# Optimization experiments

Measured on AMD Instinct MI355X. Metric: run time of the kernel, lower is better.

## Reference

```python
import jax, jax.numpy as jnp
import numpy as np

B, CIN, HIN, WIN = 1, 26, 721, 1440
K, HOUT, KH, KW = 9, 360, 9, 9
COUT = 256
PSCALE = WIN // (WIN // 2)  # lon downsample stride = 2
WOUT = WIN // 2


def setup_inputs() -> dict:
    key = jax.random.key(0)
    k1, k2, k3 = jax.random.split(key, 3)
    x = jax.random.normal(k1, (B, CIN, HIN, WIN), dtype=jnp.float32)
    # precomputed basis*quadrature stencil psi[k, ho, dh, dw] (shift-invariant in lon,
    # stored only for wo=0, exactly as DISCO does). Normalized per (k, ho) ('mean' mode).
    psi = jax.random.normal(k2, (K, HOUT, KH, KW), dtype=jnp.float32)
    psi = psi / (jnp.mean(jnp.abs(psi), axis=(2, 3), keepdims=True) * (KH * KW) + 1e-6)
    weight = jax.random.normal(k3, (COUT, CIN, K), dtype=jnp.float32) * (1.0 / np.sqrt(CIN * K))
    # base input-lat row for each output lat (stencil top row), clipped to valid range
    hi_base = np.clip(np.round(np.arange(HOUT) * (HIN - 1) / HOUT).astype(np.int32) - KH // 2, 0, HIN - 1)
    return {"x": x, "psi": psi, "weight": weight, "hi_base": jnp.asarray(hi_base, dtype=jnp.int32)}


def _disco_conv(x, psi, weight, hi_base):
    x = x.astype(jnp.float32)  # fp32 autocast-off region, matches torch module
    acc = jnp.zeros((B, CIN, K, HOUT, WOUT), dtype=jnp.float32)
    for dh in range(KH):  # small structural loop over stencil rows
        rows = jnp.clip(hi_base + dh, 0, HIN - 1)  # [Hout]
        xr = x[:, :, rows, :]
        for dw in range(KW):  # small structural loop over stencil lon offsets
            shift = dw - KW // 2
            xs = jnp.roll(xr, -shift, axis=-1)[..., ::PSCALE]  # [B,C,Hout,Wout]
            acc = acc + psi[:, :, dh, dw][None, None, :, :, None] * xs[:, :, None, :, :]
    # contract learned weights over kernel basis and input channels
    out = jnp.einsum('bckhw,ock->bohw', acc, weight)  # [B,Cout,Hout,Wout]
    return out


def reference(x, psi, weight, hi_base):
    return _disco_conv(x, psi, weight, hi_base)
```

## Files before the change

kernel.cpp:

```cpp
#include <hip/hip_runtime.h>

#define CIN_   26
#define HIN_   721
#define WIN_   1440
#define K_     9
#define HOUT_  360
#define KH_    9
#define KW_    9
#define COUT_  256
#define WOUT_  720

#define WT     16
#define XCOLS  (2*WT + 8)
#define CK     (CIN_ * K_)
#define KPAD   256
#define ACCP   264
#define NMT    (COUT_ / 16)
#define NKS    (KPAD / 32)
#define NXCD   8
#define HBAND  (HOUT_ / NXCD)

typedef short bf16x8 __attribute__((ext_vector_type(8)));
typedef float f32x4  __attribute__((ext_vector_type(4)));

__device__ unsigned short g_whi[NMT * NKS * 64 * 8];

__device__ __forceinline__ unsigned short f2bf_rne(float f) {
    union { float f; unsigned u; } v; v.f = f;
    unsigned u = v.u;
    unsigned r = (u + 0x7FFFu + ((u >> 16) & 1u)) >> 16;
    return (unsigned short)r;
}

__global__ void prep_weight_kernel(const float* __restrict__ weight) {
    const int bid  = blockIdx.x;
    const int mt   = bid / NKS;
    const int ks   = bid % NKS;
    const int lane = threadIdx.x;
    const int m    = mt * 16 + (lane & 15);
    const int k0   = ks * 32 + (lane >> 4) * 8;
    const int base = ((mt * NKS + ks) * 64 + lane) * 8;
    #pragma unroll
    for (int j = 0; j < 8; ++j) {
        const int k = k0 + j;
        const float w = (k < CK) ? weight[m * CK + k] : 0.f;
        g_whi[base + j] = f2bf_rne(w);
    }
}

__global__ __launch_bounds__(256, 4)
void disco_fused_kernel(const float* __restrict__ x,
                        const float* __restrict__ psi,
                        const int*   __restrict__ hi_base,
                        float* __restrict__ out)
{
    __shared__ unsigned short xs_bf[CK][XCOLS];
    __shared__ __align__(16) unsigned short acc_s[WT][ACCP];
    __shared__ float psi_s[K_][KH_ * KW_];

    const int b    = blockIdx.x;
    const int xcd  = b & (NXCD - 1);
    const int jb   = b >> 3;
    const int h    = xcd * HBAND + jb / 45;
    const int tile = jb % 45;
    const int w0   = tile * WT;
    const int tid  = threadIdx.x;

    const int hib = hi_base[h];

    #pragma unroll
    for (int t = 0; t < 2; ++t) {
        const int idx = tid + t * 256;
        acc_s[idx >> 5][224 + (idx & 31)] = 0;
    }

    for (int i = tid; i < K_ * KH_ * KW_; i += 256) {
        const int k  = i / 81;
        const int jj = i % 81;
        psi_s[k][jj] = psi[(k * HOUT_ + h) * 81 + jj];
    }

    const int c0 = 2 * w0 - 4;
    for (int i = tid; i < CK * XCOLS; i += 256) {
        const int col = i % XCOLS;
        const int row = i / XCOLS;
        const int dh  = row % KH_;
        const int c   = row / KH_;
        int r = hib + dh;
        if (r > HIN_ - 1) r = HIN_ - 1;
        int g = c0 + col;
        if (g < 0)      g += WIN_;
        if (g >= WIN_)  g -= WIN_;
        xs_bf[row][col] = f2bf_rne(x[((size_t)c * HIN_ + r) * WIN_ + g]);
    }
    __syncthreads();

    const int lane = tid & 63;
    const int wid  = tid >> 6;
    const int n    = lane & 15;
    const int kg   = lane >> 4;

    bf16x8 afrag[3];
    {
        const int m = n;
        #pragma unroll
        for (int ks = 0; ks < 3; ++ks) {
            union { bf16x8 v; unsigned short u[8]; } af;
            #pragma unroll
            for (int e = 0; e < 8; ++e) {
                const int s = ks * 32 + kg * 8 + e;
                float v = 0.f;
                if (m < 9) {
                    if (s < 72)      v = psi_s[m][(s >> 3) * 9 + (s & 7)];
                    else if (s < 81) v = psi_s[m][(s - 72) * 9 + 8];
                }
                af.u[e] = f2bf_rne(v);
            }
            afrag[ks] = af.v;
        }
    }

    const char* xsb = (const char*)&xs_bf[0][0];
    for (int c = wid; c < CIN_; c += 4) {
        const int base = c * (KH_ * XCOLS * 2) + 4 * n;
        f32x4 C = {0.f, 0.f, 0.f, 0.f};
        #pragma unroll
        for (int ks = 0; ks < 3; ++ks) {
            union { bf16x8 v; unsigned d[4]; unsigned short u[8]; } bf;
            if (ks < 2 || kg == 0) {
                const int dh = ks * 4 + kg;
                const char* p = xsb + base + dh * (XCOLS * 2);
                #pragma unroll
                for (int t = 0; t < 4; ++t)
                    bf.d[t] = *(const unsigned*)(p + 4 * t);
            } else if (kg == 1) {
                #pragma unroll
                for (int e = 0; e < 8; ++e)
                    bf.u[e] = *(const unsigned short*)(xsb + base + e * 80 + 16);
            } else if (kg == 2) {
                bf.d[0] = bf.d[1] = bf.d[2] = bf.d[3] = 0;
                bf.u[0] = *(const unsigned short*)(xsb + base + 8 * 80 + 16);
            } else {
                bf.d[0] = bf.d[1] = bf.d[2] = bf.d[3] = 0;
            }
            C = __builtin_amdgcn_mfma_f32_16x16x32_bf16(afrag[ks], bf.v, C, 0, 0, 0);
        }
        #pragma unroll
        for (int r = 0; r < 4; ++r) {
            const int m = kg * 4 + r;
            if (m < 9) acc_s[n][c * 9 + m] = f2bf_rne(C[r]);
        }
    }
    __syncthreads();

    f32x4 C0 = {0.f, 0.f, 0.f, 0.f};
    f32x4 C1 = C0, C2 = C0, C3 = C0;

    for (int ks = 0; ks < NKS; ++ks) {
        const int kof = ks * 32 + kg * 8;
        const bf16x8 bhi = *(const bf16x8*)&acc_s[n][kof];

        #pragma unroll
        for (int i = 0; i < 4; ++i) {
            const int mt    = wid * 4 + i;
            const int abase = ((mt * NKS + ks) * 64 + lane) * 8;
            const bf16x8 ahi = *(const bf16x8*)&g_whi[abase];
            f32x4 acc = (i == 0) ? C0 : (i == 1) ? C1 : (i == 2) ? C2 : C3;
            acc = __builtin_amdgcn_mfma_f32_16x16x32_bf16(ahi, bhi, acc, 0, 0, 0);
            if (i == 0) C0 = acc; else if (i == 1) C1 = acc; else if (i == 2) C2 = acc; else C3 = acc;
        }
    }

    #pragma unroll
    for (int i = 0; i < 4; ++i) {
        const f32x4 acc = (i == 0) ? C0 : (i == 1) ? C1 : (i == 2) ? C2 : C3;
        const int m0 = (wid * 4 + i) * 16 + kg * 4;
        #pragma unroll
        for (int r = 0; r < 4; ++r) {
            out[(size_t)(m0 + r) * (HOUT_ * WOUT_) + h * WOUT_ + w0 + n] = acc[r];
        }
    }
}

extern "C" void kernel_launch(void* const* d_in, const int* in_sizes, int n_in,
                              void* d_out, int out_size, void* d_ws, size_t ws_size,
                              hipStream_t stream)
{
    const float* x       = (const float*)d_in[0];
    const float* psi     = (const float*)d_in[1];
    const float* weight  = (const float*)d_in[2];
    const int*   hi_base = (const int*)d_in[3];
    float* out = (float*)d_out;

    hipLaunchKernelGGL(prep_weight_kernel, dim3(NMT * NKS), dim3(64), 0, stream, weight);

    dim3 grid(45 * HOUT_, 1, 1);
    dim3 block(256, 1, 1);
    hipLaunchKernelGGL(disco_fused_kernel, grid, block, 0, stream,
                       x, psi, hi_base, out);
}
```

Measured before the change: 302.6 us.

## Precompute psi MFMA fragments and vectorize x staging into padded LDS

Adds a prep kernel that converts psi into bf16 MFMA A-fragments once per output latitude, so each block loads its fragments straight from global memory instead of staging psi in LDS and converting per block. The x tile load now uses one thread per (channel, row) issuing float2 loads with packed bf16 conversion, and the LDS row pitch is changed to 42. Removing psi_s cuts LDS use, and launch bounds are raised to 5 blocks per CU to increase occupancy. In exchange, fewer threads do the x staging, which may serialize the global loads, and there is one extra small launch.

```diff
diff --git a/kernel.cpp b/kernel.cpp
--- a/kernel.cpp
+++ b/kernel.cpp
@@ -1,4 +1,5 @@
 #include <hip/hip_runtime.h>
+#include <hip/hip_bf16.h>
 
 #define CIN_   26
 #define HIN_   721
@@ -11,7 +12,7 @@
 #define WOUT_  720
 
 #define WT     16
-#define XCOLS  (2*WT + 8)
+#define XSP    42
 #define CK     (CIN_ * K_)
 #define KPAD   256
 #define ACCP   264
@@ -24,6 +25,7 @@
 typedef float f32x4  __attribute__((ext_vector_type(4)));
 
 __device__ unsigned short g_whi[NMT * NKS * 64 * 8];
+__device__ unsigned short g_pfrag[HOUT_ * 3 * 64 * 8];
 
 __device__ __forceinline__ unsigned short f2bf_rne(float f) {
     union { float f; unsigned u; } v; v.f = f;
@@ -48,15 +50,34 @@
     }
 }
 
-__global__ __launch_bounds__(256, 4)
+__global__ void prep_psi_kernel(const float* __restrict__ psi) {
+    const int h    = blockIdx.x;
+    const int lane = threadIdx.x;
+    const int m    = lane & 15;
+    const int kg   = lane >> 4;
+    #pragma unroll
+    for (int ks = 0; ks < 3; ++ks) {
+        const int base = ((h * 3 + ks) * 64 + lane) * 8;
+        #pragma unroll
+        for (int e = 0; e < 8; ++e) {
+            const int s = ks * 32 + kg * 8 + e;
+            float v = 0.f;
+            if (m < 9) {
+                if (s < 72)      v = psi[(m * HOUT_ + h) * 81 + (s >> 3) * 9 + (s & 7)];
+                else if (s < 81) v = psi[(m * HOUT_ + h) * 81 + (s - 72) * 9 + 8];
+            }
+            g_pfrag[base + e] = f2bf_rne(v);
+        }
+    }
+}
+
+__global__ __launch_bounds__(256, 5)
 void disco_fused_kernel(const float* __restrict__ x,
-                        const float* __restrict__ psi,
                         const int*   __restrict__ hi_base,
                         float* __restrict__ out)
 {
-    __shared__ unsigned short xs_bf[CK][XCOLS];
+    __shared__ unsigned short xs_bf[CK][XSP];
     __shared__ __align__(16) unsigned short acc_s[WT][ACCP];
-    __shared__ float psi_s[K_][KH_ * KW_];
 
     const int b    = blockIdx.x;
     const int xcd  = b & (NXCD - 1);
@@ -74,26 +95,24 @@
         acc_s[idx >> 5][224 + (idx & 31)] = 0;
     }
 
-    for (int i = tid; i < K_ * KH_ * KW_; i += 256) {
-        const int k  = i / 81;
-        const int jj = i % 81;
-        psi_s[k][jj] = psi[(k * HOUT_ + h) * 81 + jj];
-    }
-
     const int c0 = 2 * w0 - 4;
-    for (int i = tid; i < CK * XCOLS; i += 256) {
-        const int col = i % XCOLS;
-        const int row = i / XCOLS;
-        const int dh  = row % KH_;
-        const int c   = row / KH_;
+    if (tid < CK) {
+        const int dh = tid % KH_;
+        const int c  = tid / KH_;
         int r = hib + dh;
         if (r > HIN_ - 1) r = HIN_ - 1;
-        int g = c0 + col;
-        if (g < 0)      g += WIN_;
-        if (g >= WIN_)  g -= WIN_;
-        xs_bf[row][col] = f2bf_rne(x[((size_t)c * HIN_ + r) * WIN_ + g]);
-    }
-    __syncthreads();
+        const float* xrow = x + ((size_t)c * HIN_ + r) * WIN_;
+        unsigned short* dst = &xs_bf[tid][0];
+        #pragma unroll 4
+        for (int j = 0; j < 20; ++j) {
+            int g = c0 + 2 * j;
+            if (g < 0)          g += WIN_;
+            else if (g >= WIN_) g -= WIN_;
+            const float2 v = *reinterpret_cast<const float2*>(xrow + g);
+            const __hip_bfloat162 bv = __float22bfloat162_rn(v);
+            *reinterpret_cast<unsigned*>(dst + 2 * j) = *reinterpret_cast<const unsigned*>(&bv);
+        }
+    }
 
     const int lane = tid & 63;
     const int wid  = tid >> 6;
@@ -101,45 +120,32 @@
     const int kg   = lane >> 4;
 
     bf16x8 afrag[3];
-    {
-        const int m = n;
-        #pragma unroll
-        for (int ks = 0; ks < 3; ++ks) {
-            union { bf16x8 v; unsigned short u[8]; } af;
-            #pragma unroll
-            for (int e = 0; e < 8; ++e) {
-                const int s = ks * 32 + kg * 8 + e;
-                float v = 0.f;
-                if (m < 9) {
-                    if (s < 72)      v = psi_s[m][(s >> 3) * 9 + (s & 7)];
-                    else if (s < 81) v = psi_s[m][(s - 72) * 9 + 8];
-                }
-                af.u[e] = f2bf_rne(v);
-            }
-            afrag[ks] = af.v;
-        }
-    }
+    #pragma unroll
+    for (int ks = 0; ks < 3; ++ks)
+        afrag[ks] = *(const bf16x8*)&g_pfrag[((h * 3 + ks) * 64 + lane) * 8];
+
+    __syncthreads();
 
     const char* xsb = (const char*)&xs_bf[0][0];
     for (int c = wid; c < CIN_; c += 4) {
-        const int base = c * (KH_ * XCOLS * 2) + 4 * n;
+        const int base = c * (KH_ * XSP * 2) + 4 * n;
         f32x4 C = {0.f, 0.f, 0.f, 0.f};
         #pragma unroll
         for (int ks = 0; ks < 3; ++ks) {
             union { bf16x8 v; unsigned d[4]; unsigned short u[8]; } bf;
             if (ks < 2 || kg == 0) {
                 const int dh = ks * 4 + kg;
-                const char* p = xsb + base + dh * (XCOLS * 2);
+                const char* p = xsb + base + dh * (XSP * 2);
                 #pragma unroll
                 for (int t = 0; t < 4; ++t)
                     bf.d[t] = *(const unsigned*)(p + 4 * t);
             } else if (kg == 1) {
                 #pragma unroll
                 for (int e = 0; e < 8; ++e)
-                    bf.u[e] = *(const unsigned short*)(xsb + base + e * 80 + 16);
+                    bf.u[e] = *(const unsigned short*)(xsb + base + e * (XSP * 2) + 16);
             } else if (kg == 2) {
                 bf.d[0] = bf.d[1] = bf.d[2] = bf.d[3] = 0;
-                bf.u[0] = *(const unsigned short*)(xsb + base + 8 * 80 + 16);
+                bf.u[0] = *(const unsigned short*)(xsb + base + 8 * (XSP * 2) + 16);
             } else {
                 bf.d[0] = bf.d[1] = bf.d[2] = bf.d[3] = 0;
             }
@@ -193,9 +199,10 @@
     float* out = (float*)d_out;
 
     hipLaunchKernelGGL(prep_weight_kernel, dim3(NMT * NKS), dim3(64), 0, stream, weight);
+    hipLaunchKernelGGL(prep_psi_kernel,    dim3(HOUT_),     dim3(64), 0, stream, psi);
 
     dim3 grid(45 * HOUT_, 1, 1);
     dim3 block(256, 1, 1);
     hipLaunchKernelGGL(disco_fused_kernel, grid, block, 0, stream,
-                       x, psi, hi_base, out);
-}
+                       x, hi_base, out);
+}
```

Result: slower. 319.9 us (+5.7%).
